# Kernel tuning notes

Hardware: AMD Instinct MI355X
Metric: run time of the kernel (lower is better)

## Reference

```python
import jax, jax.numpy as jnp
import numpy as np
import math

EPS = 1e-8
IN_EPS = 1e-5  # torch F.instance_norm default eps


def _ema(x, span):
    # x: (B, S). Matches torch compute_ema: cumulative weighted sum with (1-alpha)^k weights.
    S = x.shape[1]
    alpha = 2.0 / (span + 1)
    pows = (1.0 - alpha) ** jnp.arange(S, dtype=x.dtype)  # (S,)
    scale = 1.0 / jnp.cumsum(pows)
    return jnp.cumsum(x * pows[None, :], axis=1) * scale[None, :]


def _moving_avg_replicate(a, w):
    # a: (B, L); left replicate-pad by w-1, uniform window average -> (B, L)
    p = jnp.pad(a, ((0, 0), (w - 1, 0)), mode='edge')
    cs = jnp.cumsum(p, axis=1)
    csz = jnp.concatenate([jnp.zeros_like(cs[:, :1]), cs[:, :-1]], axis=1)
    L = a.shape[1]
    return (cs[:, w - 1:] - csz[:, :L]) / w


def setup_inputs() -> dict:
    key = jax.random.key(0)
    x = jax.random.uniform(key, (131072, 24, 5), dtype=jnp.float32) + 0.1
    return {"x": x}


def reference(x):
    B, S, _ = x.shape
    open_, high, low, close, volume = [x[..., i] for i in range(5)]

    log_close = jnp.log(close + EPS)
    zcol = jnp.zeros((B, 1), dtype=x.dtype)
    returns = jnp.concatenate([zcol, log_close[:, 1:] - log_close[:, :-1]], axis=1)
    hl_ratio = (high - low) / (close + EPS)
    oc_abs = jnp.abs(open_ - close) / (close + EPS)

    close_ema3 = _ema(close, 3)
    close_ema6 = _ema(close, 6)
    close_ema12 = _ema(close, 12)
    close_ema24 = _ema(close, 24)
    vol_ema6 = _ema(volume, 6)
    vol_ema12 = _ema(volume, 12)

    t = jnp.arange(S, dtype=x.dtype)
    ang = 2.0 * math.pi * (t % 24) / 24.0
    hour_sin = jnp.broadcast_to(jnp.sin(ang)[None, :], (B, S))
    hour_cos = jnp.broadcast_to(jnp.cos(ang)[None, :], (B, S))

    momentum_3 = jnp.concatenate([jnp.zeros((B, 3), x.dtype), log_close[:, 3:] - log_close[:, :-3]], axis=1)
    momentum_6 = jnp.concatenate([jnp.zeros((B, 6), x.dtype), log_close[:, 6:] - log_close[:, :-6]], axis=1)

    # RSI over 14-step window of gains/losses of close deltas
    deltas = close[:, 1:] - close[:, :-1]
    gain = jnp.where(deltas > 0, deltas, 0.0)
    loss = jnp.where(deltas < 0, -deltas, 0.0)
    avg_gain = _moving_avg_replicate(gain, 14)
    avg_loss = _moving_avg_replicate(loss, 14)
    rs = avg_gain / (avg_loss + EPS)
    rsi = 100.0 - 100.0 / (1.0 + rs)  # (B, S-1)
    rsi = jnp.pad(rsi, ((0, 0), (1, 0)), mode='edge')  # (B, S)

    # OBV
    mult = jnp.concatenate([zcol, jnp.sign(deltas)], axis=1)
    obv = jnp.cumsum(volume * mult, axis=1)

    features = jnp.stack([
        open_, high, low, close, volume,
        returns, jnp.abs(returns), hl_ratio, oc_abs,
        close_ema3 / close, close_ema6 / close, close_ema12 / close, close_ema24 / close,
        vol_ema6 / (volume + EPS), vol_ema12 / (volume + EPS),
        jnp.log1p(volume), hour_sin, hour_cos,
        momentum_3, momentum_6,
        (close - close_ema12) / (close_ema12 + EPS),
        rsi, obv,
        jnp.broadcast_to(returns[:, -1:], (B, S)),
        jnp.broadcast_to(hl_ratio[:, -1:], (B, S)),
    ], axis=-1)  # (B, S, 25)

    features = jnp.nan_to_num(features, nan=0.0)
    # instance norm: normalize over the sequence dim per (batch, channel)
    mean = jnp.mean(features, axis=1, keepdims=True)
    var = jnp.var(features, axis=1, keepdims=True)
    return (features - mean) / jnp.sqrt(var + IN_EPS)
```

## Files before the change

### kernel.cpp

```cpp
#include <hip/hip_runtime.h>
#include <math.h>

#ifndef M_PI
#define M_PI 3.14159265358979323846
#endif

#define CTRL_ROW_SHR(n)  (0x110 | (n))
#define CTRL_ROW_BCAST15 0x142

template <int CTRL, int RM>
__device__ __forceinline__ float dpp_mov0(float v) {
  return __int_as_float(__builtin_amdgcn_update_dpp(
      0, __float_as_int(v), CTRL, RM, 0xF, true));
}

__device__ __forceinline__ float scan32_dpp(float v) {
  v += dpp_mov0<CTRL_ROW_SHR(1), 0xF>(v);
  v += dpp_mov0<CTRL_ROW_SHR(2), 0xF>(v);
  v += dpp_mov0<CTRL_ROW_SHR(4), 0xF>(v);
  v += dpp_mov0<CTRL_ROW_SHR(8), 0xF>(v);
  v += dpp_mov0<CTRL_ROW_BCAST15, 0xa>(v);
  return v;
}

__device__ __forceinline__ float shift1_dpp(float v, int s) {
  float a = dpp_mov0<CTRL_ROW_SHR(1), 0xF>(v);
  float b = dpp_mov0<CTRL_ROW_BCAST15, 0xa>(v);
  return (s == 16) ? b : a;
}

__device__ __forceinline__ void wave_lds_fence() {
  asm volatile("s_waitcnt lgkmcnt(0)" ::: "memory");
  __builtin_amdgcn_sched_barrier(0);
}

__global__ __launch_bounds__(256) void feat_in_kernel(
    const float* __restrict__ x, float* __restrict__ out, int B) {
  constexpr float EPS = 1e-8f;
  constexpr float IN_EPS = 1e-5f;

  const int tid = threadIdx.x;
  const int wave = tid >> 6;
  const int lane = tid & 63;
  const int g = lane >> 5;
  const int s = lane & 31;

  __shared__ float lds[4][1200];
  float* Lw = lds[wave];

  const long long b0 = ((long long)blockIdx.x * 4 + wave) * 2;
  long long rem = (long long)B - b0;
  int nrows = rem >= 2 ? 2 : (rem > 0 ? (int)rem : 0);

  if (nrows > 0) {
    const float4* src4 = (const float4*)(x + b0 * 120);
    float4* L4 = (float4*)Lw;
    if (lane < nrows * 30) L4[lane] = src4[lane];
  }
  wave_lds_fence();

  const bool act = (s < 24) && (g < nrows);

  int ib = g * 120 + s * 5;
  float open_ = Lw[ib + 0];
  float high  = Lw[ib + 1];
  float low   = Lw[ib + 2];
  float close = Lw[ib + 3];
  float volume= Lw[ib + 4];
  if (!act) { open_ = 0.f; high = 0.f; low = 0.f; close = 1.f; volume = 0.f; }

  float f[23];

  float lc = __logf(close + EPS);
  float lc1 = shift1_dpp(lc, s);
  float ret = (s >= 1) ? (lc - lc1) : 0.f;

  f[0] = open_; f[1] = high; f[2] = low; f[3] = close; f[4] = volume;
  f[5] = ret;   f[6] = fabsf(ret);
  float ice = 1.0f / (close + EPS);
  f[7] = (high - low) * ice;
  f[8] = fabsf(open_ - close) * ice;

  const float L2B3  = -1.0f;
  const float L2B6  = -0.48542682717024176f;
  const float L2B12 = -0.24100810933089442f;
  const float L2B24 = -0.12029423371771609f;
  float sf = (float)s;
  float w3  = exp2f(L2B3  * sf);
  float w6  = exp2f(L2B6  * sf);
  float w12 = exp2f(L2B12 * sf);
  float w24 = exp2f(L2B24 * sf);

  float e3  = scan32_dpp(close * w3 ) * (0.5f)       / (1.f - w3  * 0.5f);
  float e6  = scan32_dpp(close * w6 ) * (2.f / 7.f)  / (1.f - w6  * (5.f / 7.f));
  float e12 = scan32_dpp(close * w12) * (2.f / 13.f) / (1.f - w12 * (11.f / 13.f));
  float e24 = scan32_dpp(close * w24) * (2.f / 25.f) / (1.f - w24 * (23.f / 25.f));
  float v6  = scan32_dpp(volume * w6 ) * (2.f / 7.f)  / (1.f - w6  * (5.f / 7.f));
  float v12 = scan32_dpp(volume * w12) * (2.f / 13.f) / (1.f - w12 * (11.f / 13.f));

  float icl = 1.0f / close;
  f[9]  = e3  * icl;
  f[10] = e6  * icl;
  f[11] = e12 * icl;
  f[12] = e24 * icl;
  float iv = 1.0f / (volume + EPS);
  f[13] = v6  * iv;
  f[14] = v12 * iv;
  f[15] = __logf(1.f + volume);

  float ang = (float)(M_PI / 12.0) * sf;
  f[16] = __sinf(ang);
  f[17] = __cosf(ang);

  float lc3 = __shfl_up(lc, 3, 32);
  float lc6 = __shfl_up(lc, 6, 32);
  f[18] = (s >= 3) ? (lc - lc3) : 0.f;
  f[19] = (s >= 6) ? (lc - lc6) : 0.f;
  f[20] = (close - e12) / (e12 + EPS);

  float cl1 = shift1_dpp(close, s);
  float delta = (s >= 1) ? (close - cl1) : 0.f;
  float gain  = fmaxf(delta, 0.f);
  float lossv = fmaxf(-delta, 0.f);
  float Pg = scan32_dpp(gain);
  float Pl = scan32_dpp(lossv);
  float Pg14 = __shfl_up(Pg, 14, 32);
  float Pl14 = __shfl_up(Pl, 14, 32);
  float g1 = __shfl(gain, 1, 32);
  float l1 = __shfl(lossv, 1, 32);
  float cnt = (float)(14 - s);
  float ag = (s >= 14) ? (Pg - Pg14) : (Pg + cnt * g1);
  float al = (s >= 14) ? (Pl - Pl14) : (Pl + cnt * l1);
  ag *= (1.f / 14.f);
  al *= (1.f / 14.f);
  float rs  = ag / (al + EPS);
  float rsi = 100.f - 100.f / (1.f + rs);
  float rsi1 = __shfl(rsi, 1, 32);
  f[21] = (s == 0) ? rsi1 : rsi;

  float mult = (delta > 0.f) ? 1.f : ((delta < 0.f) ? -1.f : 0.f);
  f[22] = scan32_dpp(volume * mult);

  if (act) {
    int ob = g * 600 + s * 25;
#pragma unroll
    for (int c = 0; c < 23; c++) Lw[ob + c] = f[c];
    Lw[ob + 23] = 0.f;
    Lw[ob + 24] = 0.f;
  }
  wave_lds_fence();

  if (lane < 50) {
    int gp = lane >= 25 ? 1 : 0;
    int cp = lane - gp * 25;
    if (cp < 23 && gp < nrows) {
      float* base = Lw + gp * 600 + cp;
      float vbuf[24];
#pragma unroll
      for (int s2 = 0; s2 < 24; ++s2) vbuf[s2] = base[s2 * 25];
      float sum = 0.f;
#pragma unroll
      for (int s2 = 0; s2 < 24; ++s2) sum += vbuf[s2];
      float mean = sum * (1.f / 24.f);
      float vs = 0.f;
#pragma unroll
      for (int s2 = 0; s2 < 24; ++s2) { float d = vbuf[s2] - mean; vs += d * d; }
      float rsig = rsqrtf(vs * (1.f / 24.f) + IN_EPS);
#pragma unroll
      for (int s2 = 0; s2 < 24; ++s2) base[s2 * 25] = (vbuf[s2] - mean) * rsig;
    }
  }
  wave_lds_fence();

  if (nrows > 0) {
    float4* dst4 = (float4*)(out + b0 * 600);
    const float4* L4o = (const float4*)Lw;
    int n4 = nrows * 150;
#pragma unroll
    for (int k = lane; k < 300; k += 64) {
      if (k < n4) dst4[k] = L4o[k];
    }
  }
}

extern "C" void kernel_launch(void* const* d_in, const int* in_sizes, int n_in,
                              void* d_out, int out_size, void* d_ws, size_t ws_size,
                              hipStream_t stream) {
  const float* x = (const float*)d_in[0];
  float* out = (float*)d_out;
  int B = in_sizes[0] / 120;
  int blocks = (B + 7) / 8;
  feat_in_kernel<<<blocks, 256, 0, stream>>>(x, out, B);
}
```

Measured before the change: 78.56 us.

## Convert to persistent grid-stride kernel with register prefetch of next tile

Replaces the one-tile-per-wave launch with a persistent kernel capped at 2048 blocks, where each wave loops over tiles with a grid stride. The next tile's input is prefetched into registers while the current tile is computed, overlapping global load latency with compute. Per-lane constants (EMA weights, normalizers, hour sin/cos) are hoisted out of the loop. Risks include lower occupancy-driven latency hiding and the extra LDS fence at the end of each iteration.

```diff
diff --git a/kernel.cpp b/kernel.cpp
--- a/kernel.cpp
+++ b/kernel.cpp
@@ -35,7 +35,7 @@
 }
 
 __global__ __launch_bounds__(256) void feat_in_kernel(
-    const float* __restrict__ x, float* __restrict__ out, int B) {
+    const float* __restrict__ x, float* __restrict__ out, int B, int ntiles) {
   constexpr float EPS = 1e-8f;
   constexpr float IN_EPS = 1e-5f;
 
@@ -47,139 +47,163 @@
 
   __shared__ float lds[4][1200];
   float* Lw = lds[wave];
-
-  const long long b0 = ((long long)blockIdx.x * 4 + wave) * 2;
-  long long rem = (long long)B - b0;
-  int nrows = rem >= 2 ? 2 : (rem > 0 ? (int)rem : 0);
-
-  if (nrows > 0) {
-    const float4* src4 = (const float4*)(x + b0 * 120);
-    float4* L4 = (float4*)Lw;
-    if (lane < nrows * 30) L4[lane] = src4[lane];
-  }
-  wave_lds_fence();
-
-  const bool act = (s < 24) && (g < nrows);
-
-  int ib = g * 120 + s * 5;
-  float open_ = Lw[ib + 0];
-  float high  = Lw[ib + 1];
-  float low   = Lw[ib + 2];
-  float close = Lw[ib + 3];
-  float volume= Lw[ib + 4];
-  if (!act) { open_ = 0.f; high = 0.f; low = 0.f; close = 1.f; volume = 0.f; }
-
-  float f[23];
-
-  float lc = __logf(close + EPS);
-  float lc1 = shift1_dpp(lc, s);
-  float ret = (s >= 1) ? (lc - lc1) : 0.f;
-
-  f[0] = open_; f[1] = high; f[2] = low; f[3] = close; f[4] = volume;
-  f[5] = ret;   f[6] = fabsf(ret);
-  float ice = 1.0f / (close + EPS);
-  f[7] = (high - low) * ice;
-  f[8] = fabsf(open_ - close) * ice;
+  float4* L4 = (float4*)Lw;
 
   const float L2B3  = -1.0f;
   const float L2B6  = -0.48542682717024176f;
   const float L2B12 = -0.24100810933089442f;
   const float L2B24 = -0.12029423371771609f;
-  float sf = (float)s;
-  float w3  = exp2f(L2B3  * sf);
-  float w6  = exp2f(L2B6  * sf);
-  float w12 = exp2f(L2B12 * sf);
-  float w24 = exp2f(L2B24 * sf);
-
-  float e3  = scan32_dpp(close * w3 ) * (0.5f)       / (1.f - w3  * 0.5f);
-  float e6  = scan32_dpp(close * w6 ) * (2.f / 7.f)  / (1.f - w6  * (5.f / 7.f));
-  float e12 = scan32_dpp(close * w12) * (2.f / 13.f) / (1.f - w12 * (11.f / 13.f));
-  float e24 = scan32_dpp(close * w24) * (2.f / 25.f) / (1.f - w24 * (23.f / 25.f));
-  float v6  = scan32_dpp(volume * w6 ) * (2.f / 7.f)  / (1.f - w6  * (5.f / 7.f));
-  float v12 = scan32_dpp(volume * w12) * (2.f / 13.f) / (1.f - w12 * (11.f / 13.f));
-
-  float icl = 1.0f / close;
-  f[9]  = e3  * icl;
-  f[10] = e6  * icl;
-  f[11] = e12 * icl;
-  f[12] = e24 * icl;
-  float iv = 1.0f / (volume + EPS);
-  f[13] = v6  * iv;
-  f[14] = v12 * iv;
-  f[15] = __logf(1.f + volume);
-
-  float ang = (float)(M_PI / 12.0) * sf;
-  f[16] = __sinf(ang);
-  f[17] = __cosf(ang);
-
-  float lc3 = __shfl_up(lc, 3, 32);
-  float lc6 = __shfl_up(lc, 6, 32);
-  f[18] = (s >= 3) ? (lc - lc3) : 0.f;
-  f[19] = (s >= 6) ? (lc - lc6) : 0.f;
-  f[20] = (close - e12) / (e12 + EPS);
-
-  float cl1 = shift1_dpp(close, s);
-  float delta = (s >= 1) ? (close - cl1) : 0.f;
-  float gain  = fmaxf(delta, 0.f);
-  float lossv = fmaxf(-delta, 0.f);
-  float Pg = scan32_dpp(gain);
-  float Pl = scan32_dpp(lossv);
-  float Pg14 = __shfl_up(Pg, 14, 32);
-  float Pl14 = __shfl_up(Pl, 14, 32);
-  float g1 = __shfl(gain, 1, 32);
-  float l1 = __shfl(lossv, 1, 32);
-  float cnt = (float)(14 - s);
-  float ag = (s >= 14) ? (Pg - Pg14) : (Pg + cnt * g1);
-  float al = (s >= 14) ? (Pl - Pl14) : (Pl + cnt * l1);
-  ag *= (1.f / 14.f);
-  al *= (1.f / 14.f);
-  float rs  = ag / (al + EPS);
-  float rsi = 100.f - 100.f / (1.f + rs);
-  float rsi1 = __shfl(rsi, 1, 32);
-  f[21] = (s == 0) ? rsi1 : rsi;
-
-  float mult = (delta > 0.f) ? 1.f : ((delta < 0.f) ? -1.f : 0.f);
-  f[22] = scan32_dpp(volume * mult);
-
-  if (act) {
-    int ob = g * 600 + s * 25;
-#pragma unroll
-    for (int c = 0; c < 23; c++) Lw[ob + c] = f[c];
-    Lw[ob + 23] = 0.f;
-    Lw[ob + 24] = 0.f;
+  const float sf = (float)s;
+  const float w3  = exp2f(L2B3  * sf);
+  const float w6  = exp2f(L2B6  * sf);
+  const float w12 = exp2f(L2B12 * sf);
+  const float w24 = exp2f(L2B24 * sf);
+  const float dn3  = (0.5f)       / (1.f - w3  * 0.5f);
+  const float dn6  = (2.f / 7.f)  / (1.f - w6  * (5.f / 7.f));
+  const float dn12 = (2.f / 13.f) / (1.f - w12 * (11.f / 13.f));
+  const float dn24 = (2.f / 25.f) / (1.f - w24 * (23.f / 25.f));
+  const float ang = (float)(M_PI / 12.0) * sf;
+  const float hs = __sinf(ang);
+  const float hc = __cosf(ang);
+
+  const int tstride = gridDim.x * 4;
+  int t = blockIdx.x * 4 + wave;
+
+  float4 r4 = make_float4(0.f, 0.f, 0.f, 0.f);
+  if (t < ntiles) {
+    long long b0 = (long long)t * 2;
+    int nr = (int)(((long long)B - b0) >= 2 ? 2 : ((long long)B - b0));
+    if (lane < nr * 30) r4 = ((const float4*)(x + b0 * 120))[lane];
   }
-  wave_lds_fence();
-
-  if (lane < 50) {
-    int gp = lane >= 25 ? 1 : 0;
-    int cp = lane - gp * 25;
-    if (cp < 23 && gp < nrows) {
-      float* base = Lw + gp * 600 + cp;
-      float vbuf[24];
-#pragma unroll
-      for (int s2 = 0; s2 < 24; ++s2) vbuf[s2] = base[s2 * 25];
-      float sum = 0.f;
-#pragma unroll
-      for (int s2 = 0; s2 < 24; ++s2) sum += vbuf[s2];
-      float mean = sum * (1.f / 24.f);
-      float vs = 0.f;
-#pragma unroll
-      for (int s2 = 0; s2 < 24; ++s2) { float d = vbuf[s2] - mean; vs += d * d; }
-      float rsig = rsqrtf(vs * (1.f / 24.f) + IN_EPS);
-#pragma unroll
-      for (int s2 = 0; s2 < 24; ++s2) base[s2 * 25] = (vbuf[s2] - mean) * rsig;
-    }
-  }
-  wave_lds_fence();
-
-  if (nrows > 0) {
-    float4* dst4 = (float4*)(out + b0 * 600);
-    const float4* L4o = (const float4*)Lw;
-    int n4 = nrows * 150;
-#pragma unroll
-    for (int k = lane; k < 300; k += 64) {
-      if (k < n4) dst4[k] = L4o[k];
-    }
+
+  for (; t < ntiles; t += tstride) {
+    const long long b0 = (long long)t * 2;
+    long long rem = (long long)B - b0;
+    const int nrows = rem >= 2 ? 2 : (rem > 0 ? (int)rem : 0);
+    const bool act = (s < 24) && (g < nrows);
+
+    if (lane < nrows * 30) L4[lane] = r4;
+
+    {
+      int t2 = t + tstride;
+      if (t2 < ntiles) {
+        long long b2 = (long long)t2 * 2;
+        int nr2 = (int)(((long long)B - b2) >= 2 ? 2 : ((long long)B - b2));
+        if (lane < nr2 * 30) r4 = ((const float4*)(x + b2 * 120))[lane];
+      }
+    }
+    wave_lds_fence();
+
+    int ib = g * 120 + s * 5;
+    float open_ = Lw[ib + 0];
+    float high  = Lw[ib + 1];
+    float low   = Lw[ib + 2];
+    float close = Lw[ib + 3];
+    float volume= Lw[ib + 4];
+    if (!act) { open_ = 0.f; high = 0.f; low = 0.f; close = 1.f; volume = 0.f; }
+
+    float f[23];
+
+    float lc = __logf(close + EPS);
+    float lc1 = shift1_dpp(lc, s);
+    float ret = (s >= 1) ? (lc - lc1) : 0.f;
+
+    f[0] = open_; f[1] = high; f[2] = low; f[3] = close; f[4] = volume;
+    f[5] = ret;   f[6] = fabsf(ret);
+    float ice = 1.0f / (close + EPS);
+    f[7] = (high - low) * ice;
+    f[8] = fabsf(open_ - close) * ice;
+
+    float e3  = scan32_dpp(close * w3 ) * dn3;
+    float e6  = scan32_dpp(close * w6 ) * dn6;
+    float e12 = scan32_dpp(close * w12) * dn12;
+    float e24 = scan32_dpp(close * w24) * dn24;
+    float v6  = scan32_dpp(volume * w6 ) * dn6;
+    float v12 = scan32_dpp(volume * w12) * dn12;
+
+    float icl = 1.0f / close;
+    f[9]  = e3  * icl;
+    f[10] = e6  * icl;
+    f[11] = e12 * icl;
+    f[12] = e24 * icl;
+    float iv = 1.0f / (volume + EPS);
+    f[13] = v6  * iv;
+    f[14] = v12 * iv;
+    f[15] = __logf(1.f + volume);
+
+    f[16] = hs;
+    f[17] = hc;
+
+    float lc3 = __shfl_up(lc, 3, 32);
+    float lc6 = __shfl_up(lc, 6, 32);
+    f[18] = (s >= 3) ? (lc - lc3) : 0.f;
+    f[19] = (s >= 6) ? (lc - lc6) : 0.f;
+    f[20] = (close - e12) / (e12 + EPS);
+
+    float cl1 = shift1_dpp(close, s);
+    float delta = (s >= 1) ? (close - cl1) : 0.f;
+    float gain  = fmaxf(delta, 0.f);
+    float lossv = fmaxf(-delta, 0.f);
+    float Pg = scan32_dpp(gain);
+    float Pl = scan32_dpp(lossv);
+    float Pg14 = __shfl_up(Pg, 14, 32);
+    float Pl14 = __shfl_up(Pl, 14, 32);
+    float g1 = __shfl(gain, 1, 32);
+    float l1 = __shfl(lossv, 1, 32);
+    float cnt = (float)(14 - s);
+    float ag = (s >= 14) ? (Pg - Pg14) : (Pg + cnt * g1);
+    float al = (s >= 14) ? (Pl - Pl14) : (Pl + cnt * l1);
+    ag *= (1.f / 14.f);
+    al *= (1.f / 14.f);
+    float rs  = ag / (al + EPS);
+    float rsi = 100.f - 100.f / (1.f + rs);
+    float rsi1 = __shfl(rsi, 1, 32);
+    f[21] = (s == 0) ? rsi1 : rsi;
+
+    float mult = (delta > 0.f) ? 1.f : ((delta < 0.f) ? -1.f : 0.f);
+    f[22] = scan32_dpp(volume * mult);
+
+    if (act) {
+      int ob = g * 600 + s * 25;
+#pragma unroll
+      for (int c = 0; c < 23; c++) Lw[ob + c] = f[c];
+      Lw[ob + 23] = 0.f;
+      Lw[ob + 24] = 0.f;
+    }
+    wave_lds_fence();
+
+    if (lane < 50) {
+      int gp = lane >= 25 ? 1 : 0;
+      int cp = lane - gp * 25;
+      if (cp < 23 && gp < nrows) {
+        float* base = Lw + gp * 600 + cp;
+        float vbuf[24];
+#pragma unroll
+        for (int s2 = 0; s2 < 24; ++s2) vbuf[s2] = base[s2 * 25];
+        float sum = 0.f;
+#pragma unroll
+        for (int s2 = 0; s2 < 24; ++s2) sum += vbuf[s2];
+        float mean = sum * (1.f / 24.f);
+        float vs = 0.f;
+#pragma unroll
+        for (int s2 = 0; s2 < 24; ++s2) { float d = vbuf[s2] - mean; vs += d * d; }
+        float rsig = rsqrtf(vs * (1.f / 24.f) + IN_EPS);
+#pragma unroll
+        for (int s2 = 0; s2 < 24; ++s2) base[s2 * 25] = (vbuf[s2] - mean) * rsig;
+      }
+    }
+    wave_lds_fence();
+
+    if (nrows > 0) {
+      float4* dst4 = (float4*)(out + b0 * 600);
+      const float4* L4o = (const float4*)Lw;
+      int n4 = nrows * 150;
+#pragma unroll
+      for (int k = lane; k < 300; k += 64) {
+        if (k < n4) dst4[k] = L4o[k];
+      }
+    }
+    wave_lds_fence();
   }
 }
 
@@ -189,6 +213,8 @@
   const float* x = (const float*)d_in[0];
   float* out = (float*)d_out;
   int B = in_sizes[0] / 120;
-  int blocks = (B + 7) / 8;
-  feat_in_kernel<<<blocks, 256, 0, stream>>>(x, out, B);
-}
+  int ntiles = (B + 1) / 2;
+  int blocks_needed = (ntiles + 3) / 4;
+  int blocks = blocks_needed < 2048 ? blocks_needed : 2048;
+  feat_in_kernel<<<blocks, 256, 0, stream>>>(x, out, B, ntiles);
+}
```

Result: slower. 88.71 us (+12.9%).
